# Optimization experiments

Measured on AMD Instinct MI355X. Metric: run time of the kernel, lower is better.

Reference implementation:

```python
import jax, jax.numpy as jnp
import numpy as np

N_NODES = 245760      # 8192 graphs * 30 atoms
N_GRAPHS = 8192
N_EDGES = 1000000
NODES_PER_GRAPH = 30
F_NODE = 78
F_CELL = 1000
HID = 64


def _lin(key, fan_in, fan_out):
    kw, kb = jax.random.split(key)
    s = 1.0 / np.sqrt(fan_in)
    W = jax.random.uniform(kw, (fan_in, fan_out), minval=-s, maxval=s, dtype=jnp.float32)
    b = jax.random.uniform(kb, (fan_out,), minval=-s, maxval=s, dtype=jnp.float32)
    return W, b


def setup_inputs() -> dict:
    key = jax.random.key(0)
    ks = jax.random.split(key, 14)
    x = jax.random.normal(ks[0], (N_NODES, F_NODE), dtype=jnp.float32)
    # edges constrained within each graph: node = graph_id * 30 + local offset
    offs = jax.random.randint(ks[1], (2, N_EDGES), 0, NODES_PER_GRAPH)
    ge = jax.random.randint(ks[2], (N_EDGES,), 0, N_GRAPHS)
    edge_index = (ge[None, :] * NODES_PER_GRAPH + offs).astype(jnp.int64)
    batch = jnp.repeat(jnp.arange(N_GRAPHS, dtype=jnp.int64), NODES_PER_GRAPH)
    cell_features = jax.random.normal(ks[3], (N_GRAPHS, F_CELL), dtype=jnp.float32)
    W1, b1 = _lin(ks[4], F_NODE, HID)
    W2, b2 = _lin(ks[5], HID, 2 * HID)
    W3, b3 = _lin(ks[6], 2 * HID, 4 * HID)
    Wd, bd = _lin(ks[7], 4 * HID, HID)          # drug_embed_fc
    Wc1, bc1 = _lin(ks[8], F_CELL, 2 * HID)      # cell_fc1
    Wc2, bc2 = _lin(ks[9], 2 * HID, HID)         # cell_fc2
    Wm1, bm1 = _lin(ks[10], 2 * HID, HID)        # combiner_fc1
    Wm2, bm2 = _lin(ks[11], HID, 32)             # combiner_fc2
    Wo, bo = _lin(ks[12], 32, 1)                 # output_fc
    return {"x": x, "edge_index": edge_index, "batch": batch,
            "cell_features": cell_features,
            "W1": W1, "b1": b1, "W2": W2, "b2": b2, "W3": W3, "b3": b3,
            "Wd": Wd, "bd": bd, "Wc1": Wc1, "bc1": bc1, "Wc2": Wc2, "bc2": bc2,
            "Wm1": Wm1, "bm1": bm1, "Wm2": Wm2, "bm2": bm2, "Wo": Wo, "bo": bo}


def _gcn_conv(h, W, b, srcA, dstA, norm, n_nodes):
    # PyG GCNConv: linear transform, then sym-normalized scatter-add (self-loops included in srcA/dstA/norm)
    h = h @ W                                   # [N, out]
    msg = h[srcA] * norm[:, None]               # gather + edge scaling
    out = jnp.zeros((n_nodes, W.shape[1]), h.dtype).at[dstA].add(msg)
    return out + b


def reference(x, edge_index, batch, cell_features,
              W1, b1, W2, b2, W3, b3, Wd, bd,
              Wc1, bc1, Wc2, bc2, Wm1, bm1, Wm2, bm2, Wo, bo):
    n = x.shape[0]
    loops = jnp.arange(n, dtype=edge_index.dtype)
    srcA = jnp.concatenate([edge_index[0], loops])
    dstA = jnp.concatenate([edge_index[1], loops])
    deg = jax.ops.segment_sum(jnp.ones_like(dstA, dtype=x.dtype), dstA, num_segments=n)
    dinv = jax.lax.rsqrt(deg)                   # deg >= 1 due to self-loops
    norm = dinv[srcA] * dinv[dstA]

    h = jax.nn.relu(_gcn_conv(x, W1, b1, srcA, dstA, norm, n))
    h = jax.nn.relu(_gcn_conv(h, W2, b2, srcA, dstA, norm, n))
    h = jax.nn.relu(_gcn_conv(h, W3, b3, srcA, dstA, norm, n))

    # global mean pool over graphs
    sums = jax.ops.segment_sum(h, batch, num_segments=N_GRAPHS)
    cnts = jax.ops.segment_sum(jnp.ones((n,), h.dtype), batch, num_segments=N_GRAPHS)
    drug = (sums / cnts[:, None]) @ Wd + bd     # [B, HID]

    cell = jax.nn.relu(cell_features @ Wc1 + bc1)
    cell = cell @ Wc2 + bc2                      # [B, HID]

    comb = jnp.concatenate([drug, cell], axis=1)
    z = jax.nn.relu(comb @ Wm1 + bm1)
    z = jax.nn.relu(z @ Wm2 + bm2)
    out = z @ Wo + bo
    return out.reshape(-1)
```

## Files before the change

kernel.cpp:

```cpp
#include <hip/hip_runtime.h>

typedef __attribute__((ext_vector_type(8))) short short8;
typedef __attribute__((ext_vector_type(4))) short short4v;
typedef __attribute__((ext_vector_type(4))) float f32x4;
typedef unsigned short u16;

__device__ __forceinline__ u16 f2bf(float f) {
    union { float f; unsigned u; } v; v.f = f;
    unsigned r = v.u + 0x7FFFu + ((v.u >> 16) & 1u);
    return (u16)(r >> 16);
}
__device__ __forceinline__ float bf2f(u16 h) {
    union { unsigned u; float f; } v; v.u = ((unsigned)h) << 16;
    return v.f;
}
__device__ __forceinline__ void split2(float f, u16& h, u16& l) {
    h = f2bf(f);
    l = f2bf(f - bf2f(h));
}
__device__ __forceinline__ short8 ld8(const u16* p) {
    short4v a = *(const short4v*)p;
    short4v b = *(const short4v*)(p + 4);
    short8 r;
    r[0] = a[0]; r[1] = a[1]; r[2] = a[2]; r[3] = a[3];
    r[4] = b[0]; r[5] = b[1]; r[6] = b[2]; r[7] = b[3];
    return r;
}
#define MFMA(A, B, C) __builtin_amdgcn_mfma_f32_16x16x32_bf16(A, B, C, 0, 0, 0)


__global__ void k_zero4(int4* __restrict__ p, int n4) {
    int i = blockIdx.x * 256 + threadIdx.x;
    if (i < n4) p[i] = make_int4(0, 0, 0, 0);
}

__global__ void k_cnt(const int* __restrict__ ei, int* __restrict__ Acnt, int E) {
    int e = blockIdx.x * 256 + threadIdx.x;
    if (e >= E) return;
    int s = ei[e], d = ei[E + e];
    int g = d / 30;
    atomicAdd(&Acnt[(size_t)g * 960 + (d - g * 30) * 32 + (s - g * 30)], 1);
}

__global__ void k_split_t(const float* __restrict__ W, u16* __restrict__ th,
                          u16* __restrict__ tl, int K, int F, int Kp) {
    int idx = blockIdx.x * 256 + threadIdx.x;
    if (idx >= F * Kp) return;
    int f = idx / Kp, k = idx % Kp;
    float v = (k < K) ? W[(size_t)k * F + f] : 0.f;
    u16 h, l; split2(v, h, l);
    th[idx] = h; tl[idx] = l;
}

__global__ void k_split_rows(const float* __restrict__ cf, u16* __restrict__ o, int B) {
    int idx = blockIdx.x * 256 + threadIdx.x;
    if (idx >= B * 1024) return;
    int r = idx >> 10, c = idx & 1023;
    float v = (c < 1000) ? cf[(size_t)r * 1000 + c] : 0.f;
    u16 h, l; split2(v, h, l);
    o[(size_t)r * 2048 + c] = h;
    o[(size_t)r * 2048 + 1024 + c] = l;
}

__global__ __launch_bounds__(512, 6) void k_node(
    const float* __restrict__ x, const int* __restrict__ Acnt,
    const u16* __restrict__ W1h, const u16* __restrict__ W1l,
    const u16* __restrict__ W2h, const u16* __restrict__ W2l,
    const u16* __restrict__ W3h, const u16* __restrict__ W3l,
    const float* __restrict__ b1, const float* __restrict__ b2,
    const float* __restrict__ b3, float* __restrict__ P) {
    __shared__ __align__(16) char smem[46976];
    u16* xh  = (u16*)(smem + 0);
    u16* xl  = (u16*)(smem + 6400);
    u16* h1h = (u16*)(smem + 0);
    u16* h1l = (u16*)(smem + 4352);
    u16* a3h = (u16*)(smem + 0);
    u16* a3l = (u16*)(smem + 8448);
    u16* t1h = (u16*)(smem + 16896);
    u16* t1l = (u16*)(smem + 21504);
    u16* h2h = (u16*)(smem + 16896);
    u16* h2l = (u16*)(smem + 26112);
    float* Afp  = (float*)(smem + 35328);
    u16* Ah  = (u16*)(smem + 39424);
    u16* Al  = (u16*)(smem + 41728);
    float* dv   = (float*)(smem + 44032);
    float* pool = (float*)(smem + 44160);
    float* bias = (float*)(smem + 45184);

    int t = threadIdx.x;
    int g = blockIdx.x;
    int wave = t >> 6, lane = t & 63, quad = lane >> 4, l15 = lane & 15;

    {
        uint* zp = (uint*)smem;
        for (int i = t; i < 3200; i += 512) zp[i] = 0;
        if (t < 448) bias[t] = (t < 64) ? b1[t] : (t < 192 ? b2[t - 64] : b3[t - 192]);
    }
    __syncthreads();
    {
        const float4* xg = (const float4*)(x + (size_t)g * 2340);
        for (int i = t; i < 585; i += 512) {
            float4 v = xg[i];
            int base = i * 4;
            float vv[4] = {v.x, v.y, v.z, v.w};
#pragma unroll
            for (int j = 0; j < 4; j++) {
                int idx = base + j;
                int r = idx / 78, c = idx - r * 78;
                u16 h, l; split2(vv[j], h, l);
                xh[r * 100 + c] = h; xl[r * 100 + c] = l;
            }
        }
        const int* ac = Acnt + (size_t)g * 960;
        for (int i = t; i < 960; i += 512) Afp[i] = (float)ac[i];
    }
    __syncthreads();
    if (t < 32) {
        float s = 0.f;
        if (t < 30)
            for (int j = 0; j < 32; j++) s += Afp[t * 32 + j];
        dv[t] = (t < 30) ? rsqrtf(s + 1.f) : 0.f;
    }
    __syncthreads();
    {
        for (int i = t; i < 960; i += 512) {
            int r = i >> 5, c = i & 31;
            float a = (Afp[i] + (r == c ? 1.f : 0.f)) * dv[r] * dv[c];
            u16 h, l; split2(a, h, l);
            Ah[r * 36 + c] = h; Al[r * 36 + c] = l;
        }
        if (t < 64) {
            int r = 30 + (t >> 5), c = t & 31;
            Ah[r * 36 + c] = 0; Al[r * 36 + c] = 0;
        }
    }
    __syncthreads();
    {
        int wm = wave >> 2, wn = wave & 3;
        int arow = wm * 16 + l15;
        int col = wn * 16 + l15;
        const u16* wph = W1h + col * 96 + quad * 8;
        const u16* wpl = W1l + col * 96 + quad * 8;
        f32x4 acc = {0.f, 0.f, 0.f, 0.f};
#pragma unroll
        for (int ch = 0; ch < 3; ch++) {
            int kc = ch * 32;
            short8 bh = *(const short8*)(wph + kc);
            short8 bl = *(const short8*)(wpl + kc);
            short8 ah = ld8(&xh[arow * 100 + kc + quad * 8]);
            short8 al = ld8(&xl[arow * 100 + kc + quad * 8]);
            acc = MFMA(ah, bh, acc);
            acc = MFMA(al, bh, acc);
            acc = MFMA(ah, bl, acc);
        }
#pragma unroll
        for (int rg = 0; rg < 4; rg++) {
            int row = wm * 16 + quad * 4 + rg;
            u16 h, l; split2(acc[rg], h, l);
            t1h[col * 36 + row] = h;
            t1l[col * 36 + row] = l;
        }
    }
    __syncthreads();
    {
        int wm = wave >> 2, wn = wave & 3;
        int arow = wm * 16 + l15;
        int col = wn * 16 + l15;
        short8 aAh = ld8(&Ah[arow * 36 + quad * 8]);
        short8 aAl = ld8(&Al[arow * 36 + quad * 8]);
        short8 bh = ld8(&t1h[col * 36 + quad * 8]);
        short8 bl = ld8(&t1l[col * 36 + quad * 8]);
        f32x4 acc = {0.f, 0.f, 0.f, 0.f};
        acc = MFMA(aAh, bh, acc);
        acc = MFMA(aAl, bh, acc);
        acc = MFMA(aAh, bl, acc);
        float bb = bias[col];
#pragma unroll
        for (int rg = 0; rg < 4; rg++) {
            int row = wm * 16 + quad * 4 + rg;
            float v = fmaxf(acc[rg] + bb, 0.f);
            u16 h, l; split2(v, h, l);
            h1h[row * 68 + col] = h;
            h1l[row * 68 + col] = l;
        }
    }
    __syncthreads();
    {
        int col = wave * 16 + l15;
        const u16* wph = W2h + col * 64 + quad * 8;
        const u16* wpl = W2l + col * 64 + quad * 8;
        f32x4 acc[2] = {{0.f,0.f,0.f,0.f},{0.f,0.f,0.f,0.f}};
#pragma unroll
        for (int ch = 0; ch < 2; ch++) {
            int kc = ch * 32;
            short8 bh = *(const short8*)(wph + kc);
            short8 bl = *(const short8*)(wpl + kc);
#pragma unroll
            for (int mi = 0; mi < 2; mi++) {
                short8 ah = ld8(&h1h[(mi * 16 + l15) * 68 + kc + quad * 8]);
                short8 al = ld8(&h1l[(mi * 16 + l15) * 68 + kc + quad * 8]);
                acc[mi] = MFMA(ah, bh, acc[mi]);
                acc[mi] = MFMA(al, bh, acc[mi]);
                acc[mi] = MFMA(ah, bl, acc[mi]);
            }
        }
        float bb = bias[64 + col];
#pragma unroll
        for (int mi = 0; mi < 2; mi++)
#pragma unroll
            for (int rg = 0; rg < 4; rg++) {
                int row = mi * 16 + quad * 4 + rg;
                float v = fmaxf(acc[mi][rg] + bb, 0.f);
                u16 h, l; split2(v, h, l);
                h2h[col * 36 + row] = h;
                h2l[col * 36 + row] = l;
            }
    }
    __syncthreads();
    {
        int col = wave * 16 + l15;
        short8 bh = ld8(&h2h[col * 36 + quad * 8]);
        short8 bl = ld8(&h2l[col * 36 + quad * 8]);
        f32x4 acc[2] = {{0.f,0.f,0.f,0.f},{0.f,0.f,0.f,0.f}};
#pragma unroll
        for (int mi = 0; mi < 2; mi++) {
            short8 aAh = ld8(&Ah[(mi * 16 + l15) * 36 + quad * 8]);
            short8 aAl = ld8(&Al[(mi * 16 + l15) * 36 + quad * 8]);
            acc[mi] = MFMA(aAh, bh, acc[mi]);
            acc[mi] = MFMA(aAl, bh, acc[mi]);
            acc[mi] = MFMA(aAh, bl, acc[mi]);
        }
#pragma unroll
        for (int mi = 0; mi < 2; mi++)
#pragma unroll
            for (int rg = 0; rg < 4; rg++) {
                int row = mi * 16 + quad * 4 + rg;
                u16 h, l; split2(acc[mi][rg], h, l);
                a3h[row * 132 + col] = h;
                a3l[row * 132 + col] = l;
            }
    }
    __syncthreads();
    {
        int colb = wave * 32;
        f32x4 acc[2][2] = {{{0.f,0.f,0.f,0.f},{0.f,0.f,0.f,0.f}},
                           {{0.f,0.f,0.f,0.f},{0.f,0.f,0.f,0.f}}};
        short8 cwh[2], cwl[2], nwh[2], nwl[2];
#pragma unroll
        for (int ni = 0; ni < 2; ni++) {
            size_t o = (size_t)(colb + ni * 16 + l15) * 128 + quad * 8;
            cwh[ni] = *(const short8*)(W3h + o);
            cwl[ni] = *(const short8*)(W3l + o);
        }
#pragma unroll
        for (int ch = 0; ch < 4; ch++) {
            if (ch < 3) {
#pragma unroll
                for (int ni = 0; ni < 2; ni++) {
                    size_t o = (size_t)(colb + ni * 16 + l15) * 128 + (ch + 1) * 32 + quad * 8;
                    nwh[ni] = *(const short8*)(W3h + o);
                    nwl[ni] = *(const short8*)(W3l + o);
                }
            }
            short8 ah[2], al[2];
#pragma unroll
            for (int mi = 0; mi < 2; mi++) {
                ah[mi] = ld8(&a3h[(mi * 16 + l15) * 132 + ch * 32 + quad * 8]);
                al[mi] = ld8(&a3l[(mi * 16 + l15) * 132 + ch * 32 + quad * 8]);
            }
#pragma unroll
            for (int mi = 0; mi < 2; mi++)
#pragma unroll
                for (int ni = 0; ni < 2; ni++) {
                    acc[mi][ni] = MFMA(ah[mi], cwh[ni], acc[mi][ni]);
                    acc[mi][ni] = MFMA(al[mi], cwh[ni], acc[mi][ni]);
                    acc[mi][ni] = MFMA(ah[mi], cwl[ni], acc[mi][ni]);
                }
            if (ch < 3) {
#pragma unroll
                for (int ni = 0; ni < 2; ni++) { cwh[ni] = nwh[ni]; cwl[ni] = nwl[ni]; }
            }
        }
#pragma unroll
        for (int ni = 0; ni < 2; ni++) {
            int col = colb + ni * 16 + l15;
            float bb = bias[192 + col];
            float p = 0.f;
#pragma unroll
            for (int mi = 0; mi < 2; mi++)
#pragma unroll
                for (int rg = 0; rg < 4; rg++) {
                    int row = mi * 16 + quad * 4 + rg;
                    if (row < 30) p += fmaxf(acc[mi][ni][rg] + bb, 0.f);
                }
            p += __shfl_down(p, 32);
            p += __shfl_down(p, 16);
            if (lane < 16) pool[colb + ni * 16 + lane] = p;
        }
    }
    __syncthreads();
    if (t < 256) P[(size_t)g * 256 + t] = pool[t] * (1.0f / 30.0f);
}

template<int NT>
__global__ __launch_bounds__(256) void k_mgemm(const u16* __restrict__ Xs,
        const u16* __restrict__ Wth, const u16* __restrict__ Wtl,
        const float* __restrict__ bias, float* __restrict__ Y,
        int K, int Kp, int F) {
    const int BN = NT * 32;
    __shared__ __align__(16) u16 Xh_l[128 * 40];
    __shared__ __align__(16) u16 Xl_l[128 * 40];
    __shared__ __align__(16) u16 Wh_l[BN * 40];
    __shared__ __align__(16) u16 Wl_l[BN * 40];
    int t = threadIdx.x;
    int row0 = blockIdx.x * 128, col0 = blockIdx.y * BN;
    int wave = t >> 6, lane = t & 63, quad = lane >> 4, l15 = lane & 15;
    int wm = wave >> 1, wn = wave & 1;
    f32x4 acc[4][NT];
#pragma unroll
    for (int mi = 0; mi < 4; mi++)
#pragma unroll
        for (int ni = 0; ni < NT; ni++)
#pragma unroll
            for (int q = 0; q < 4; q++) acc[mi][ni][q] = 0.f;

    int nch = Kp >> 5;
    for (int ch = 0; ch < nch; ch++) {
        int kc = ch << 5;
#pragma unroll
        for (int i = 0; i < 4; i++) {
            int f4 = t + i * 256, r = f4 >> 3, c4 = f4 & 7;
            const u16* rp = Xs + (size_t)(row0 + r) * (2 * K) + kc + c4 * 4;
            *(ushort4*)&Xh_l[r * 40 + c4 * 4] = *(const ushort4*)rp;
            *(ushort4*)&Xl_l[r * 40 + c4 * 4] = *(const ushort4*)(rp + K);
        }
#pragma unroll
        for (int i = 0; i < BN / 32; i++) {
            int f4 = t + i * 256, n = f4 >> 3, c4 = f4 & 7;
            size_t go = (size_t)(col0 + n) * Kp + kc + c4 * 4;
            *(ushort4*)&Wh_l[n * 40 + c4 * 4] = *(const ushort4*)(Wth + go);
            *(ushort4*)&Wl_l[n * 40 + c4 * 4] = *(const ushort4*)(Wtl + go);
        }
        __syncthreads();
        short8 ah[4], al[4], bh[NT], bl[NT];
#pragma unroll
        for (int mi = 0; mi < 4; mi++) {
            int r = wm * 64 + mi * 16 + l15;
            ah[mi] = *(const short8*)&Xh_l[r * 40 + quad * 8];
            al[mi] = *(const short8*)&Xl_l[r * 40 + quad * 8];
        }
#pragma unroll
        for (int ni = 0; ni < NT; ni++) {
            int c = wn * (BN / 2) + ni * 16 + l15;
            bh[ni] = *(const short8*)&Wh_l[c * 40 + quad * 8];
            bl[ni] = *(const short8*)&Wl_l[c * 40 + quad * 8];
        }
#pragma unroll
        for (int mi = 0; mi < 4; mi++)
#pragma unroll
            for (int ni = 0; ni < NT; ni++) {
                acc[mi][ni] = MFMA(ah[mi], bh[ni], acc[mi][ni]);
                acc[mi][ni] = MFMA(al[mi], bh[ni], acc[mi][ni]);
                acc[mi][ni] = MFMA(ah[mi], bl[ni], acc[mi][ni]);
            }
        __syncthreads();
    }
#pragma unroll
    for (int mi = 0; mi < 4; mi++) {
        int row = row0 + wm * 64 + mi * 16 + quad * 4;
#pragma unroll
        for (int ni = 0; ni < NT; ni++) {
            int col = col0 + wn * (BN / 2) + ni * 16 + l15;
            float bv = bias[col];
#pragma unroll
            for (int rg = 0; rg < 4; rg++)
                Y[(size_t)(row + rg) * F + col] = fmaxf(acc[mi][ni][rg] + bv, 0.f);
        }
    }
}

__global__ __launch_bounds__(256) void k_tail(const float* __restrict__ pooled,
        const float* __restrict__ cell1,
        const float* __restrict__ Wd, const float* __restrict__ bd,
        const float* __restrict__ Wc2, const float* __restrict__ bc2,
        const float* __restrict__ Wm1, const float* __restrict__ bm1,
        const float* __restrict__ Wm2, const float* __restrict__ bm2,
        const float* __restrict__ Wo, const float* __restrict__ bo,
        float* __restrict__ out) {
    __shared__ float pr[1024];
    __shared__ float c1[512];
    __shared__ float dz[512];
    __shared__ float z1f[256];
    __shared__ float z2f[128];
    int t = threadIdx.x;
    int g0 = blockIdx.x * 4;
    int gl = t >> 6, c = t & 63;
    ((float4*)pr)[t] = ((const float4*)(pooled + (size_t)g0 * 256))[t];
    if (t < 128) ((float4*)c1)[t] = ((const float4*)(cell1 + (size_t)g0 * 128))[t];
    __syncthreads();
    float s = bd[c];
#pragma unroll 8
    for (int k = 0; k < 256; k++) s += pr[gl * 256 + k] * Wd[k * 64 + c];
    dz[gl * 128 + c] = s;
    float s2 = bc2[c];
#pragma unroll 8
    for (int k = 0; k < 128; k++) s2 += c1[gl * 128 + k] * Wc2[k * 64 + c];
    dz[gl * 128 + 64 + c] = s2;
    __syncthreads();
    float s3 = bm1[c];
#pragma unroll 8
    for (int k = 0; k < 128; k++) s3 += dz[gl * 128 + k] * Wm1[k * 64 + c];
    z1f[gl * 64 + c] = fmaxf(s3, 0.f);
    __syncthreads();
    if (c < 32) {
        float s4 = bm2[c];
#pragma unroll 8
        for (int k = 0; k < 64; k++) s4 += z1f[gl * 64 + k] * Wm2[k * 32 + c];
        z2f[gl * 32 + c] = fmaxf(s4, 0.f);
    }
    __syncthreads();
    float v = (c < 32) ? z2f[gl * 32 + c] * Wo[c] : 0.f;
#pragma unroll
    for (int off = 32; off > 0; off >>= 1) v += __shfl_down(v, off);
    if (c == 0) out[g0 + gl] = v + bo[0];
}


extern "C" void kernel_launch(void* const* d_in, const int* in_sizes, int n_in,
                              void* d_out, int out_size, void* d_ws, size_t ws_size,
                              hipStream_t stream) {
    const float* x   = (const float*)d_in[0];
    const int*   ei  = (const int*)d_in[1];
    const float* cf  = (const float*)d_in[3];
    const float* W1  = (const float*)d_in[4];
    const float* b1  = (const float*)d_in[5];
    const float* W2  = (const float*)d_in[6];
    const float* b2  = (const float*)d_in[7];
    const float* W3  = (const float*)d_in[8];
    const float* b3  = (const float*)d_in[9];
    const float* Wd  = (const float*)d_in[10];
    const float* bd  = (const float*)d_in[11];
    const float* Wc1 = (const float*)d_in[12];
    const float* bc1 = (const float*)d_in[13];
    const float* Wc2 = (const float*)d_in[14];
    const float* bc2 = (const float*)d_in[15];
    const float* Wm1 = (const float*)d_in[16];
    const float* bm1 = (const float*)d_in[17];
    const float* Wm2 = (const float*)d_in[18];
    const float* bm2 = (const float*)d_in[19];
    const float* Wo  = (const float*)d_in[20];
    const float* bo  = (const float*)d_in[21];
    float* out = (float*)d_out;

    const int E = in_sizes[1] / 2;
    const int B = in_sizes[3] / 1000;

    char* w = (char*)d_ws;
    auto carve = [&](size_t bytes) { void* p = (void*)w; w += (bytes + 255) & ~(size_t)255; return p; };
    int*   Acnt   = (int*)  carve((size_t)B * 960 * 4);
    float* pooled = (float*)carve((size_t)B * 256 * 4);
    float* cell1  = (float*)carve((size_t)B * 128 * 4);
    u16* W1th = (u16*)carve(64 * 96 * 2);     u16* W1tl = (u16*)carve(64 * 96 * 2);
    u16* W2th = (u16*)carve(128 * 64 * 2);    u16* W2tl = (u16*)carve(128 * 64 * 2);
    u16* W3th = (u16*)carve(256 * 128 * 2);   u16* W3tl = (u16*)carve(256 * 128 * 2);
    u16* Wc1th = (u16*)carve(128 * 1024 * 2); u16* Wc1tl = (u16*)carve(128 * 1024 * 2);
    u16* cfs = (u16*)carve((size_t)B * 2048 * 2);

    auto g1 = [](int n) { return (n + 255) / 256; };

    k_zero4<<<g1(B * 240), 256, 0, stream>>>((int4*)Acnt, B * 240);
    k_cnt<<<g1(E), 256, 0, stream>>>(ei, Acnt, E);

    k_split_t<<<g1(64 * 96), 256, 0, stream>>>(W1, W1th, W1tl, 78, 64, 96);
    k_split_t<<<g1(128 * 64), 256, 0, stream>>>(W2, W2th, W2tl, 64, 128, 64);
    k_split_t<<<g1(256 * 128), 256, 0, stream>>>(W3, W3th, W3tl, 128, 256, 128);
    k_split_t<<<g1(128 * 1024), 256, 0, stream>>>(Wc1, Wc1th, Wc1tl, 1000, 128, 1024);
    k_split_rows<<<g1(B * 1024), 256, 0, stream>>>(cf, cfs, B);

    k_node<<<B, 512, 0, stream>>>(x, Acnt,
                                  W1th, W1tl, W2th, W2tl, W3th, W3tl,
                                  b1, b2, b3, pooled);

    k_mgemm<1><<<dim3(B / 128, 4), 256, 0, stream>>>(cfs, Wc1th, Wc1tl, bc1, cell1, 1024, 1024, 128);

    k_tail<<<B / 4, 256, 0, stream>>>(pooled, cell1, Wd, bd, Wc2, bc2,
                                      Wm1, bm1, Wm2, bm2, Wo, bo, out);
}
```

Baseline: 497.5 us.

## Pack adjacency counts to 16-bit, fuse cell-feature split into GEMM, trim node-kernel LDS

Adjacency edge counts are now packed two per 32-bit word with shifted atomics, which halves the count buffer and the bytes to zero and read. The separate cell-feature bf16 split pass and its scratch buffer are removed, and a new k_cell kernel loads the fp32 features, splits them in LDS, and does the 1000->128 GEMM in 32-row tiles with weights read straight from global. The node kernel drops its LDS bias and pool buffers, writes pooled results directly, merges the degree computation into the load phase to save barriers, and zeros only the padding, so LDS falls and the occupancy hint rises to 8. The risks are 16-bit count overflow if many edges repeat one pair, and uncached weight reads in k_cell.

```diff
diff --git a/kernel.cpp b/kernel.cpp
--- a/kernel.cpp
+++ b/kernel.cpp
@@ -34,12 +34,13 @@
     if (i < n4) p[i] = make_int4(0, 0, 0, 0);
 }
 
-__global__ void k_cnt(const int* __restrict__ ei, int* __restrict__ Acnt, int E) {
+__global__ void k_cnt(const int* __restrict__ ei, unsigned* __restrict__ A32, int E) {
     int e = blockIdx.x * 256 + threadIdx.x;
     if (e >= E) return;
     int s = ei[e], d = ei[E + e];
     int g = d / 30;
-    atomicAdd(&Acnt[(size_t)g * 960 + (d - g * 30) * 32 + (s - g * 30)], 1);
+    int idx = g * 960 + (d - g * 30) * 32 + (s - g * 30);
+    atomicAdd(&A32[idx >> 1], 1u << ((idx & 1) * 16));
 }
 
 __global__ void k_split_t(const float* __restrict__ W, u16* __restrict__ th,
@@ -52,52 +53,42 @@
     th[idx] = h; tl[idx] = l;
 }
 
-__global__ void k_split_rows(const float* __restrict__ cf, u16* __restrict__ o, int B) {
-    int idx = blockIdx.x * 256 + threadIdx.x;
-    if (idx >= B * 1024) return;
-    int r = idx >> 10, c = idx & 1023;
-    float v = (c < 1000) ? cf[(size_t)r * 1000 + c] : 0.f;
-    u16 h, l; split2(v, h, l);
-    o[(size_t)r * 2048 + c] = h;
-    o[(size_t)r * 2048 + 1024 + c] = l;
-}
-
-__global__ __launch_bounds__(512, 6) void k_node(
-    const float* __restrict__ x, const int* __restrict__ Acnt,
+__global__ __launch_bounds__(512, 8) void k_node(
+    const float* __restrict__ x, const unsigned* __restrict__ A32,
     const u16* __restrict__ W1h, const u16* __restrict__ W1l,
     const u16* __restrict__ W2h, const u16* __restrict__ W2l,
     const u16* __restrict__ W3h, const u16* __restrict__ W3l,
     const float* __restrict__ b1, const float* __restrict__ b2,
     const float* __restrict__ b3, float* __restrict__ P) {
-    __shared__ __align__(16) char smem[46976];
+    __shared__ __align__(16) char smem[39936];
     u16* xh  = (u16*)(smem + 0);
     u16* xl  = (u16*)(smem + 6400);
     u16* h1h = (u16*)(smem + 0);
     u16* h1l = (u16*)(smem + 4352);
     u16* a3h = (u16*)(smem + 0);
     u16* a3l = (u16*)(smem + 8448);
+    float* Afp = (float*)(smem + 16896);
+    float* dv  = (float*)(smem + 20736);
     u16* t1h = (u16*)(smem + 16896);
     u16* t1l = (u16*)(smem + 21504);
     u16* h2h = (u16*)(smem + 16896);
     u16* h2l = (u16*)(smem + 26112);
-    float* Afp  = (float*)(smem + 35328);
-    u16* Ah  = (u16*)(smem + 39424);
-    u16* Al  = (u16*)(smem + 41728);
-    float* dv   = (float*)(smem + 44032);
-    float* pool = (float*)(smem + 44160);
-    float* bias = (float*)(smem + 45184);
+    u16* Ah  = (u16*)(smem + 35328);
+    u16* Al  = (u16*)(smem + 37632);
 
     int t = threadIdx.x;
     int g = blockIdx.x;
     int wave = t >> 6, lane = t & 63, quad = lane >> 4, l15 = lane & 15;
 
     {
-        uint* zp = (uint*)smem;
-        for (int i = t; i < 3200; i += 512) zp[i] = 0;
-        if (t < 448) bias[t] = (t < 64) ? b1[t] : (t < 192 ? b2[t - 64] : b3[t - 192]);
-    }
-    __syncthreads();
-    {
+        for (int i = t; i < 860; i += 512) {
+            uint* arr = (uint*)((i >= 430) ? (char*)xl : (char*)xh);
+            int j = (i >= 430) ? i - 430 : i;
+            int r, c32;
+            if (j < 330) { r = j / 11; c32 = 39 + j % 11; }
+            else { r = 30 + (j - 330) / 50; c32 = (j - 330) % 50; }
+            arr[r * 50 + c32] = 0;
+        }
         const float4* xg = (const float4*)(x + (size_t)g * 2340);
         for (int i = t; i < 585; i += 512) {
             float4 v = xg[i];
@@ -111,27 +102,35 @@
                 xh[r * 100 + c] = h; xl[r * 100 + c] = l;
             }
         }
-        const int* ac = Acnt + (size_t)g * 960;
-        for (int i = t; i < 960; i += 512) Afp[i] = (float)ac[i];
-    }
-    __syncthreads();
-    if (t < 32) {
-        float s = 0.f;
-        if (t < 30)
-            for (int j = 0; j < 32; j++) s += Afp[t * 32 + j];
-        dv[t] = (t < 30) ? rsqrtf(s + 1.f) : 0.f;
-    }
-    __syncthreads();
-    {
-        for (int i = t; i < 960; i += 512) {
+        const unsigned* ac = A32 + (size_t)g * 480;
+        for (int i = t; i < 480; i += 512) {
+            unsigned w = ac[i];
+            Afp[2 * i] = (float)(w & 0xFFFFu);
+            Afp[2 * i + 1] = (float)(w >> 16);
+        }
+        if (t < 32) {
+            float s = 1.f;
+            if (t < 30) {
+                const unsigned* rp = ac + t * 16;
+                unsigned acc = 0;
+#pragma unroll
+                for (int j = 0; j < 16; j++) { unsigned w = rp[j]; acc += (w & 0xFFFFu) + (w >> 16); }
+                s += (float)acc;
+            }
+            dv[t] = (t < 30) ? rsqrtf(s) : 0.f;
+        }
+    }
+    __syncthreads();
+    {
+#pragma unroll
+        for (int ii = 0; ii < 2; ii++) {
+            int i = t + ii * 512;
             int r = i >> 5, c = i & 31;
-            float a = (Afp[i] + (r == c ? 1.f : 0.f)) * dv[r] * dv[c];
+            float a = 0.f;
+            if (r < 30 && c < 30)
+                a = (Afp[r * 32 + c] + (r == c ? 1.f : 0.f)) * dv[r] * dv[c];
             u16 h, l; split2(a, h, l);
             Ah[r * 36 + c] = h; Al[r * 36 + c] = l;
-        }
-        if (t < 64) {
-            int r = 30 + (t >> 5), c = t & 31;
-            Ah[r * 36 + c] = 0; Al[r * 36 + c] = 0;
         }
     }
     __syncthreads();
@@ -174,7 +173,7 @@
         acc = MFMA(aAh, bh, acc);
         acc = MFMA(aAl, bh, acc);
         acc = MFMA(aAh, bl, acc);
-        float bb = bias[col];
+        float bb = b1[col];
 #pragma unroll
         for (int rg = 0; rg < 4; rg++) {
             int row = wm * 16 + quad * 4 + rg;
@@ -204,7 +203,7 @@
                 acc[mi] = MFMA(ah, bl, acc[mi]);
             }
         }
-        float bb = bias[64 + col];
+        float bb = b2[col];
 #pragma unroll
         for (int mi = 0; mi < 2; mi++)
 #pragma unroll
@@ -284,7 +283,7 @@
 #pragma unroll
         for (int ni = 0; ni < 2; ni++) {
             int col = colb + ni * 16 + l15;
-            float bb = bias[192 + col];
+            float bb = b3[col];
             float p = 0.f;
 #pragma unroll
             for (int mi = 0; mi < 2; mi++)
@@ -295,87 +294,75 @@
                 }
             p += __shfl_down(p, 32);
             p += __shfl_down(p, 16);
-            if (lane < 16) pool[colb + ni * 16 + lane] = p;
-        }
-    }
-    __syncthreads();
-    if (t < 256) P[(size_t)g * 256 + t] = pool[t] * (1.0f / 30.0f);
-}
-
-template<int NT>
-__global__ __launch_bounds__(256) void k_mgemm(const u16* __restrict__ Xs,
+            if (lane < 16)
+                P[(size_t)g * 256 + colb + ni * 16 + lane] = p * (1.0f / 30.0f);
+        }
+    }
+}
+
+__global__ __launch_bounds__(256) void k_cell(const float* __restrict__ cf,
         const u16* __restrict__ Wth, const u16* __restrict__ Wtl,
-        const float* __restrict__ bias, float* __restrict__ Y,
-        int K, int Kp, int F) {
-    const int BN = NT * 32;
-    __shared__ __align__(16) u16 Xh_l[128 * 40];
-    __shared__ __align__(16) u16 Xl_l[128 * 40];
-    __shared__ __align__(16) u16 Wh_l[BN * 40];
-    __shared__ __align__(16) u16 Wl_l[BN * 40];
+        const float* __restrict__ bias, float* __restrict__ Y) {
+    __shared__ __align__(16) u16 Xh[32 * 136];
+    __shared__ __align__(16) u16 Xl[32 * 136];
     int t = threadIdx.x;
-    int row0 = blockIdx.x * 128, col0 = blockIdx.y * BN;
+    int row0 = blockIdx.x * 32;
     int wave = t >> 6, lane = t & 63, quad = lane >> 4, l15 = lane & 15;
-    int wm = wave >> 1, wn = wave & 1;
-    f32x4 acc[4][NT];
-#pragma unroll
-    for (int mi = 0; mi < 4; mi++)
-#pragma unroll
-        for (int ni = 0; ni < NT; ni++)
-#pragma unroll
-            for (int q = 0; q < 4; q++) acc[mi][ni][q] = 0.f;
-
-    int nch = Kp >> 5;
-    for (int ch = 0; ch < nch; ch++) {
-        int kc = ch << 5;
-#pragma unroll
-        for (int i = 0; i < 4; i++) {
-            int f4 = t + i * 256, r = f4 >> 3, c4 = f4 & 7;
-            const u16* rp = Xs + (size_t)(row0 + r) * (2 * K) + kc + c4 * 4;
-            *(ushort4*)&Xh_l[r * 40 + c4 * 4] = *(const ushort4*)rp;
-            *(ushort4*)&Xl_l[r * 40 + c4 * 4] = *(const ushort4*)(rp + K);
-        }
-#pragma unroll
-        for (int i = 0; i < BN / 32; i++) {
-            int f4 = t + i * 256, n = f4 >> 3, c4 = f4 & 7;
-            size_t go = (size_t)(col0 + n) * Kp + kc + c4 * 4;
-            *(ushort4*)&Wh_l[n * 40 + c4 * 4] = *(const ushort4*)(Wth + go);
-            *(ushort4*)&Wl_l[n * 40 + c4 * 4] = *(const ushort4*)(Wtl + go);
+    f32x4 acc[2][2] = {{{0.f,0.f,0.f,0.f},{0.f,0.f,0.f,0.f}},
+                       {{0.f,0.f,0.f,0.f},{0.f,0.f,0.f,0.f}}};
+    for (int ko = 0; ko < 8; ko++) {
+#pragma unroll
+        for (int ii = 0; ii < 4; ii++) {
+            int i = t + ii * 256;
+            int r = i >> 5, c4 = i & 31;
+            int col = ko * 128 + c4 * 4;
+            float4 v = {0.f, 0.f, 0.f, 0.f};
+            if (col < 1000) v = *(const float4*)(cf + (size_t)(row0 + r) * 1000 + col);
+            float vv[4] = {v.x, v.y, v.z, v.w};
+#pragma unroll
+            for (int j = 0; j < 4; j++) {
+                u16 h, l; split2(vv[j], h, l);
+                Xh[r * 136 + c4 * 4 + j] = h;
+                Xl[r * 136 + c4 * 4 + j] = l;
+            }
         }
         __syncthreads();
-        short8 ah[4], al[4], bh[NT], bl[NT];
-#pragma unroll
-        for (int mi = 0; mi < 4; mi++) {
-            int r = wm * 64 + mi * 16 + l15;
-            ah[mi] = *(const short8*)&Xh_l[r * 40 + quad * 8];
-            al[mi] = *(const short8*)&Xl_l[r * 40 + quad * 8];
-        }
-#pragma unroll
-        for (int ni = 0; ni < NT; ni++) {
-            int c = wn * (BN / 2) + ni * 16 + l15;
-            bh[ni] = *(const short8*)&Wh_l[c * 40 + quad * 8];
-            bl[ni] = *(const short8*)&Wl_l[c * 40 + quad * 8];
-        }
-#pragma unroll
-        for (int mi = 0; mi < 4; mi++)
-#pragma unroll
-            for (int ni = 0; ni < NT; ni++) {
-                acc[mi][ni] = MFMA(ah[mi], bh[ni], acc[mi][ni]);
-                acc[mi][ni] = MFMA(al[mi], bh[ni], acc[mi][ni]);
-                acc[mi][ni] = MFMA(ah[mi], bl[ni], acc[mi][ni]);
-            }
+#pragma unroll
+        for (int kk = 0; kk < 4; kk++) {
+            int klo = kk * 32 + quad * 8;
+            short8 ah[2], al[2];
+#pragma unroll
+            for (int mi = 0; mi < 2; mi++) {
+                ah[mi] = ld8(&Xh[(mi * 16 + l15) * 136 + klo]);
+                al[mi] = ld8(&Xl[(mi * 16 + l15) * 136 + klo]);
+            }
+#pragma unroll
+            for (int ni = 0; ni < 2; ni++) {
+                int col = wave * 32 + ni * 16 + l15;
+                size_t o = (size_t)col * 1024 + ko * 128 + kk * 32 + quad * 8;
+                short8 bh = *(const short8*)(Wth + o);
+                short8 bl = *(const short8*)(Wtl + o);
+#pragma unroll
+                for (int mi = 0; mi < 2; mi++) {
+                    acc[mi][ni] = MFMA(ah[mi], bh, acc[mi][ni]);
+                    acc[mi][ni] = MFMA(al[mi], bh, acc[mi][ni]);
+                    acc[mi][ni] = MFMA(ah[mi], bl, acc[mi][ni]);
+                }
+            }
+        }
         __syncthreads();
     }
 #pragma unroll
-    for (int mi = 0; mi < 4; mi++) {
-        int row = row0 + wm * 64 + mi * 16 + quad * 4;
-#pragma unroll
-        for (int ni = 0; ni < NT; ni++) {
-            int col = col0 + wn * (BN / 2) + ni * 16 + l15;
-            float bv = bias[col];
-#pragma unroll
-            for (int rg = 0; rg < 4; rg++)
-                Y[(size_t)(row + rg) * F + col] = fmaxf(acc[mi][ni][rg] + bv, 0.f);
-        }
+    for (int ni = 0; ni < 2; ni++) {
+        int col = wave * 32 + ni * 16 + l15;
+        float bv = bias[col];
+#pragma unroll
+        for (int mi = 0; mi < 2; mi++)
+#pragma unroll
+            for (int rg = 0; rg < 4; rg++) {
+                int row = row0 + mi * 16 + quad * 4 + rg;
+                Y[(size_t)row * 128 + col] = fmaxf(acc[mi][ni][rg] + bv, 0.f);
+            }
     }
 }
 
@@ -457,31 +444,29 @@
 
     char* w = (char*)d_ws;
     auto carve = [&](size_t bytes) { void* p = (void*)w; w += (bytes + 255) & ~(size_t)255; return p; };
-    int*   Acnt   = (int*)  carve((size_t)B * 960 * 4);
+    unsigned* A32 = (unsigned*)carve((size_t)B * 960 * 2);
     float* pooled = (float*)carve((size_t)B * 256 * 4);
     float* cell1  = (float*)carve((size_t)B * 128 * 4);
     u16* W1th = (u16*)carve(64 * 96 * 2);     u16* W1tl = (u16*)carve(64 * 96 * 2);
     u16* W2th = (u16*)carve(128 * 64 * 2);    u16* W2tl = (u16*)carve(128 * 64 * 2);
     u16* W3th = (u16*)carve(256 * 128 * 2);   u16* W3tl = (u16*)carve(256 * 128 * 2);
     u16* Wc1th = (u16*)carve(128 * 1024 * 2); u16* Wc1tl = (u16*)carve(128 * 1024 * 2);
-    u16* cfs = (u16*)carve((size_t)B * 2048 * 2);
 
     auto g1 = [](int n) { return (n + 255) / 256; };
 
-    k_zero4<<<g1(B * 240), 256, 0, stream>>>((int4*)Acnt, B * 240);
-    k_cnt<<<g1(E), 256, 0, stream>>>(ei, Acnt, E);
+    k_zero4<<<g1(B * 120), 256, 0, stream>>>((int4*)A32, B * 120);
+    k_cnt<<<g1(E), 256, 0, stream>>>(ei, A32, E);
 
     k_split_t<<<g1(64 * 96), 256, 0, stream>>>(W1, W1th, W1tl, 78, 64, 96);
     k_split_t<<<g1(128 * 64), 256, 0, stream>>>(W2, W2th, W2tl, 64, 128, 64);
     k_split_t<<<g1(256 * 128), 256, 0, stream>>>(W3, W3th, W3tl, 128, 256, 128);
     k_split_t<<<g1(128 * 1024), 256, 0, stream>>>(Wc1, Wc1th, Wc1tl, 1000, 128, 1024);
-    k_split_rows<<<g1(B * 1024), 256, 0, stream>>>(cf, cfs, B);
-
-    k_node<<<B, 512, 0, stream>>>(x, Acnt,
+
+    k_node<<<B, 512, 0, stream>>>(x, A32,
                                   W1th, W1tl, W2th, W2tl, W3th, W3tl,
                                   b1, b2, b3, pooled);
 
-    k_mgemm<1><<<dim3(B / 128, 4), 256, 0, stream>>>(cfs, Wc1th, Wc1tl, bc1, cell1, 1024, 1024, 128);
+    k_cell<<<B / 32, 256, 0, stream>>>(cf, Wc1th, Wc1tl, bc1, cell1);
 
     k_tail<<<B / 4, 256, 0, stream>>>(pooled, cell1, Wd, bd, Wc2, bc2,
                                       Wm1, bm1, Wm2, bm2, Wo, bo, out);
```

Result: faster. 476.5 us (-4.2%).
